# Optimization experiments

Measured on AMD Instinct MI355X. Metric: run time of the kernel, lower is better.

## Reference

```python
import jax, jax.numpy as jnp
import numpy as np

HEADS = 8
DIM_HEAD = 64
DIM_COOR = 3
SCALE = (DIM_COOR * DIM_HEAD) ** -0.5


def setup_inputs() -> dict:
    key = jax.random.key(0)
    k1, k2, k3 = jax.random.split(key, 3)
    x = jax.random.normal(k1, (2, 2048, 256, 3), dtype=jnp.float32)
    w_qkv = jax.random.normal(k2, (1536, 256), dtype=jnp.float32)
    w_out = jax.random.normal(k3, (256, 512), dtype=jnp.float32)
    return {"x": x, "w_qkv": w_qkv, "w_out": w_out}


def reference(x, w_qkv, w_out):
    b, n, _, c = x.shape
    # VNLinear: contract feature dim, keep coord dim  -> [b, n, 3*h*d, c]
    qkv = jnp.einsum('bnic,oi->bnoc', x, w_qkv)
    q, k, v = jnp.split(qkv, 3, axis=-2)  # each [b, n, h*d, c]

    def to_heads(t):
        return t.reshape(b, n, HEADS, DIM_HEAD, c).transpose(0, 2, 1, 3, 4)  # b h n d c

    q, k, v = map(to_heads, (q, k, v))
    q = q * SCALE
    # scores sum over head-dim AND coordinate-dim
    sim = jnp.einsum('bhidc,bhjdc->bhij', q, k)
    attn = jax.nn.softmax(sim, axis=-1)
    out = jnp.einsum('bhij,bhjdc->bhidc', attn, v)  # coord dim preserved
    out = out.transpose(0, 2, 1, 3, 4).reshape(b, n, HEADS * DIM_HEAD, c)
    return jnp.einsum('bnic,oi->bnoc', out, w_out)
```

## Files before the change

kernel.cpp:

```cpp
#include <hip/hip_runtime.h>
#include <hip/hip_bf16.h>

#define SCALE 0.07216878364870322f
#define LOG2E 1.4426950408889634f

typedef __bf16 bf16x8 __attribute__((ext_vector_type(8)));
typedef float f32x16 __attribute__((ext_vector_type(16)));
typedef float f32x4v __attribute__((ext_vector_type(4)));
typedef unsigned int u32x4 __attribute__((ext_vector_type(4)));
typedef unsigned short u16;

#define MFMA(a, b, c) __builtin_amdgcn_mfma_f32_32x32x16_bf16(a, b, c, 0, 0, 0)
#define MFMA16(a, b, c) __builtin_amdgcn_mfma_f32_16x16x32_bf16(a, b, c, 0, 0, 0)

__device__ __forceinline__ u16 b16(float v) { return __builtin_bit_cast(u16, (__bf16)v); }
__device__ __forceinline__ float fb16(u16 u) {
    unsigned int t = (unsigned int)u << 16;
    return __builtin_bit_cast(float, t);
}
__device__ __forceinline__ unsigned int splitpack(float v) {
    u16 h = b16(v);
    float r = v - fb16(h);
    return (unsigned int)h | ((unsigned int)b16(r) << 16);
}
__device__ __forceinline__ unsigned int pack2(float a, float b) {
    return (unsigned int)b16(a) | ((unsigned int)b16(b) << 16);
}
__device__ __forceinline__ void gload16(const void* g, void* l) {
    __builtin_amdgcn_global_load_lds((const __attribute__((address_space(1))) void*)g,
                                     (__attribute__((address_space(3))) void*)l, 16, 0, 0);
}

__global__ __launch_bounds__(256) void qkv_mfma(const float* __restrict__ x,
                                                const float* __restrict__ wq,
                                                u16* __restrict__ Qhi, u16* __restrict__ Qlo,
                                                u16* __restrict__ KVf) {
    __shared__ unsigned int ldsr[2][32][196];
    const int tid = threadIdx.x;
    const int lane = tid & 63, w = tid >> 6, hf = lane >> 5, l31 = lane & 31;
    const int lq = lane & 15, gq = lane >> 4;
    const int o0 = blockIdx.x * 64;
    const int n0 = blockIdx.y * 128;
    const int b = blockIdx.z;
    const int nw0 = n0 + w * 32;
    const int part = o0 >> 9;
    const int h = (o0 >> 6) & 7;
    const int bh = b * 8 + h;

    const float* xp = x + ((size_t)(b * 2048 + nw0 + l31)) * 768 + hf * 24;
    const float* wp0 = wq + (size_t)(o0 + l31) * 256 + hf * 8;
    const float* wp1 = wp0 + 32 * 256;

    f32x16 acc[3][2] = {};
    #pragma unroll 2
    for (int k0 = 0; k0 < 16; ++k0) {
        float xf[24], wf0[8], wf1[8];
        #pragma unroll
        for (int q = 0; q < 6; ++q) {
            f32x4v t = *(const f32x4v*)(xp + k0 * 48 + q * 4);
            xf[q * 4 + 0] = t[0]; xf[q * 4 + 1] = t[1];
            xf[q * 4 + 2] = t[2]; xf[q * 4 + 3] = t[3];
        }
        {
            f32x4v t0 = *(const f32x4v*)(wp0 + k0 * 16);
            f32x4v t1 = *(const f32x4v*)(wp0 + k0 * 16 + 4);
            f32x4v t2 = *(const f32x4v*)(wp1 + k0 * 16);
            f32x4v t3 = *(const f32x4v*)(wp1 + k0 * 16 + 4);
            #pragma unroll
            for (int e = 0; e < 4; ++e) {
                wf0[e] = t0[e]; wf0[4 + e] = t1[e];
                wf1[e] = t2[e]; wf1[4 + e] = t3[e];
            }
        }
        bf16x8 xh[3], xl[3], wh[2], wl[2];
        #pragma unroll
        for (int c = 0; c < 3; ++c)
            #pragma unroll
            for (int e = 0; e < 8; ++e) {
                float v = xf[e * 3 + c];
                __bf16 hi = (__bf16)v;
                xh[c][e] = hi;
                xl[c][e] = (__bf16)(v - (float)hi);
            }
        #pragma unroll
        for (int e = 0; e < 8; ++e) {
            { float v = wf0[e]; __bf16 hi = (__bf16)v; wh[0][e] = hi; wl[0][e] = (__bf16)(v - (float)hi); }
            { float v = wf1[e]; __bf16 hi = (__bf16)v; wh[1][e] = hi; wl[1][e] = (__bf16)(v - (float)hi); }
        }
        #pragma unroll
        for (int c = 0; c < 3; ++c)
            #pragma unroll
            for (int ot = 0; ot < 2; ++ot) {
                acc[c][ot] = MFMA(xh[c], wh[ot], acc[c][ot]);
                acc[c][ot] = MFMA(xl[c], wh[ot], acc[c][ot]);
                acc[c][ot] = MFMA(xh[c], wl[ot], acc[c][ot]);
            }
    }

    #pragma unroll
    for (int round = 0; round < 2; ++round) {
        __syncthreads();
        if ((w >> 1) == round) {
            unsigned int (*L)[196] = ldsr[w & 1];
            #pragma unroll
            for (int c = 0; c < 3; ++c)
                #pragma unroll
                for (int ot = 0; ot < 2; ++ot)
                    #pragma unroll
                    for (int r = 0; r < 16; ++r) {
                        float v = acc[c][ot][r];
                        if (part == 0) v *= (SCALE * LOG2E);
                        int nn = (r & 3) + 8 * (r >> 2) + 4 * hf;
                        int dcol = 3 * (ot * 32 + l31) + c;
                        L[nn][dcol] = (part == 2) ? (unsigned int)b16(v) : splitpack(v);
                    }
            if (part < 2) {
                #pragma unroll
                for (int is = 0; is < 2; ++is)
                    #pragma unroll
                    for (int kc = 0; kc < 6; ++kc) {
                        const unsigned int* p = &L[is * 16 + lq][kc * 32 + gq * 8];
                        u32x4 a = *(const u32x4*)p;
                        u32x4 bq = *(const u32x4*)(p + 4);
                        u32x4 hi = { (a[0] & 0xffffu) | (a[1] << 16), (a[2] & 0xffffu) | (a[3] << 16),
                                     (bq[0] & 0xffffu) | (bq[1] << 16), (bq[2] & 0xffffu) | (bq[3] << 16) };
                        u32x4 lo = { (a[0] >> 16) | (a[1] & 0xffff0000u), (a[2] >> 16) | (a[3] & 0xffff0000u),
                                     (bq[0] >> 16) | (bq[1] & 0xffff0000u), (bq[2] >> 16) | (bq[3] & 0xffff0000u) };
                        if (part == 0) {
                            size_t off = ((size_t)(bh * 128 + (nw0 >> 4) + is) * 6 + kc) * 512 + lane * 8;
                            *(u32x4*)(Qhi + off) = hi;
                            *(u32x4*)(Qlo + off) = lo;
                        } else {
                            size_t off = (size_t)(bh * 64 + (nw0 >> 5)) * 18432 + (is * 6 + kc) * 512 + lane * 8;
                            *(u32x4*)(KVf + off) = hi;
                            *(u32x4*)(KVf + off + 6144) = lo;
                        }
                    }
            } else {
                u16* vp = KVf + (size_t)(bh * 64 + (nw0 >> 5)) * 18432 + 12288 + lane * 8;
                #pragma unroll
                for (int d = 0; d < 12; ++d) {
                    unsigned int t[8];
                    #pragma unroll
                    for (int e = 0; e < 8; ++e)
                        t[e] = L[gq * 8 + e][d * 16 + lq];
                    u32x4 pk = { (t[0] & 0xffffu) | (t[1] << 16), (t[2] & 0xffffu) | (t[3] << 16),
                                 (t[4] & 0xffffu) | (t[5] << 16), (t[6] & 0xffffu) | (t[7] << 16) };
                    *(u32x4*)(vp + d * 512) = pk;
                }
            }
        }
    }
}

__global__ __launch_bounds__(256, 2) void attn_mfma(
    const u16* __restrict__ Qhi, const u16* __restrict__ Qlo,
    const u16* __restrict__ KVf, u16* __restrict__ Opart, float* __restrict__ MLp) {
    __shared__ __align__(16) u16 lds[2][18432];
    const int tid = threadIdx.x;
    const int lane = tid & 63;
    const int w = tid >> 6;
    const int g = lane >> 4;
    const int i = lane & 15;
    const int id = blockIdx.x;
    const int rem = id >> 3;
    const int grp = ((rem >> 4) << 3) | (id & 7);
    const int itile = rem & 15;
    const int bh = grp >> 1;
    const int half = grp & 1;

    bf16x8 qh[2][6], ql[2][6];
    #pragma unroll
    for (int is = 0; is < 2; ++is) {
        size_t qb = (size_t)(bh * 128 + itile * 8 + w * 2 + is) * 3072 + (size_t)lane * 8;
        #pragma unroll
        for (int kc = 0; kc < 6; ++kc) {
            qh[is][kc] = *(const bf16x8*)(Qhi + qb + kc * 512);
            ql[is][kc] = *(const bf16x8*)(Qlo + qb + kc * 512);
        }
    }

    const char* gKV = (const char*)KVf + (size_t)bh * 2359296;
    auto stage = [&](int buf, int jtAbs) {
        const char* src = gKV + (size_t)jtAbs * 36864;
        char* dst = (char*)&lds[buf][0];
        #pragma unroll
        for (int s = 0; s < 9; ++s) {
            const int c16 = (tid + s * 256) * 16;
            gload16(src + c16, dst + c16);
        }
    };

    const int jt0 = half * 32;
    stage(0, jt0);
    __syncthreads();
    int cur = 0;

    f32x4v o[2][12] = {};
    float m_run[2] = {-1e30f, -1e30f}, l_run[2] = {0.f, 0.f};

    for (int t = 0; t < 32; ++t) {
        if (t + 1 < 32) stage(cur ^ 1, jt0 + t + 1);
        const u16* L = &lds[cur][0];

        f32x4v s4[2][2] = {};
        __builtin_amdgcn_s_setprio(1);
        #pragma unroll
        for (int kc = 0; kc < 6; ++kc) {
            bf16x8 kh0 = *(const bf16x8*)&L[(unsigned)(kc * 512) + lane * 8];
            bf16x8 kh1 = *(const bf16x8*)&L[(unsigned)((6 + kc) * 512) + lane * 8];
            bf16x8 kl0 = *(const bf16x8*)&L[6144u + (unsigned)(kc * 512) + lane * 8];
            bf16x8 kl1 = *(const bf16x8*)&L[6144u + (unsigned)((6 + kc) * 512) + lane * 8];
            s4[0][0] = MFMA16(kh0, qh[0][kc], s4[0][0]);
            s4[0][1] = MFMA16(kh1, qh[0][kc], s4[0][1]);
            s4[1][0] = MFMA16(kh0, qh[1][kc], s4[1][0]);
            s4[1][1] = MFMA16(kh1, qh[1][kc], s4[1][1]);
            s4[0][0] = MFMA16(kh0, ql[0][kc], s4[0][0]);
            s4[0][1] = MFMA16(kh1, ql[0][kc], s4[0][1]);
            s4[1][0] = MFMA16(kh0, ql[1][kc], s4[1][0]);
            s4[1][1] = MFMA16(kh1, ql[1][kc], s4[1][1]);
            s4[0][0] = MFMA16(kl0, qh[0][kc], s4[0][0]);
            s4[0][1] = MFMA16(kl1, qh[0][kc], s4[0][1]);
            s4[1][0] = MFMA16(kl0, qh[1][kc], s4[1][0]);
            s4[1][1] = MFMA16(kl1, qh[1][kc], s4[1][1]);
        }
        __builtin_amdgcn_s_setprio(0);

        bf16x8 pb[2];
        #pragma unroll
        for (int is = 0; is < 2; ++is) {
            float pm = -1e30f;
            #pragma unroll
            for (int js = 0; js < 2; ++js)
                #pragma unroll
                for (int r = 0; r < 4; ++r) pm = fmaxf(pm, s4[is][js][r]);
            pm = fmaxf(pm, __shfl_xor(pm, 16, 64));
            pm = fmaxf(pm, __shfl_xor(pm, 32, 64));
            if (!__all(pm <= m_run[is] + 8.0f)) {
                float mnew = fmaxf(m_run[is], pm);
                float sc = exp2f(m_run[is] - mnew);
                l_run[is] *= sc;
                #pragma unroll
                for (int d = 0; d < 12; ++d) o[is][d] = o[is][d] * sc;
                m_run[is] = mnew;
            }
            float rs = 0.f;
            unsigned int w0[2], w1[2];
            #pragma unroll
            for (int js = 0; js < 2; ++js) {
                float p0 = exp2f(s4[is][js][0] - m_run[is]), p1 = exp2f(s4[is][js][1] - m_run[is]);
                float p2 = exp2f(s4[is][js][2] - m_run[is]), p3 = exp2f(s4[is][js][3] - m_run[is]);
                rs += (p0 + p1) + (p2 + p3);
                w0[js] = pack2(p0, p1);
                w1[js] = pack2(p2, p3);
            }
            rs += __shfl_xor(rs, 16, 64);
            rs += __shfl_xor(rs, 32, 64);
            l_run[is] += rs;

            u32x4 F;
            const int slA = ((g & 1) << 5) + i;
            const int slB = slA + 16;
            const bool ghi = (g >> 1) != 0;
            { unsigned a0 = __shfl((int)w0[0], slA, 64), a1 = __shfl((int)w0[1], slA, 64); F[0] = ghi ? a1 : a0; }
            { unsigned a0 = __shfl((int)w1[0], slA, 64), a1 = __shfl((int)w1[1], slA, 64); F[1] = ghi ? a1 : a0; }
            { unsigned a0 = __shfl((int)w0[0], slB, 64), a1 = __shfl((int)w0[1], slB, 64); F[2] = ghi ? a1 : a0; }
            { unsigned a0 = __shfl((int)w1[0], slB, 64), a1 = __shfl((int)w1[1], slB, 64); F[3] = ghi ? a1 : a0; }
            pb[is] = __builtin_bit_cast(bf16x8, F);
        }

        __builtin_amdgcn_s_setprio(1);
        #pragma unroll
        for (int d = 0; d < 12; ++d) {
            bf16x8 vf = *(const bf16x8*)&L[12288u + (unsigned)(d * 512) + lane * 8];
            o[0][d] = MFMA16(vf, pb[0], o[0][d]);
            o[1][d] = MFMA16(vf, pb[1], o[1][d]);
        }
        __builtin_amdgcn_s_setprio(0);

        if (t + 1 < 32) {
            __syncthreads();
            cur ^= 1;
        }
    }

    #pragma unroll
    for (int is = 0; is < 2; ++is) {
        const int tI = bh * 128 + itile * 8 + w * 2 + is;
        u16* Op = Opart + (size_t)(half * 2048 + tI) * 3072 + lane;
        #pragma unroll
        for (int d = 0; d < 12; ++d)
            #pragma unroll
            for (int r = 0; r < 4; ++r)
                Op[(d * 4 + r) * 64] = b16(o[is][d][r]);
        float* mlp = MLp + (size_t)(half * 2048 + tI) * 128 + lane * 2;
        mlp[0] = m_run[is];
        mlp[1] = l_run[is];
    }
}

__global__ __launch_bounds__(256) void attn_combine(const u16* __restrict__ Opart,
                                                    const float* __restrict__ MLp,
                                                    unsigned int* __restrict__ att2) {
    const int tid = threadIdx.x, lane = tid & 63, w = tid >> 6;
    const int g = lane >> 4, i = lane & 15;
    const int tI = blockIdx.x * 4 + w;
    const int bh = tI >> 7;
    const float* mla = MLp + (size_t)tI * 128 + lane * 2;
    const float* mlb = MLp + (size_t)(2048 + tI) * 128 + lane * 2;
    float ma = mla[0], la = mla[1];
    float mb = mlb[0], lb = mlb[1];
    float mm = fmaxf(ma, mb);
    float wa = exp2f(ma - mm), wb = exp2f(mb - mm);
    float inv = 1.0f / (la * wa + lb * wb);
    const u16* Oa = Opart + (size_t)tI * 3072 + lane;
    const u16* Ob = Opart + (size_t)(2048 + tI) * 3072 + lane;
    const int b2 = bh >> 3, hh = bh & 7;
    const int ig = (tI & 127) * 16 + i;
    const int itq = ig >> 5, i31 = ig & 31;
    #pragma unroll
    for (int d = 0; d < 12; ++d)
        #pragma unroll
        for (int r = 0; r < 4; ++r) {
            float va = fb16(Oa[(d * 4 + r) * 64]);
            float vb = fb16(Ob[(d * 4 + r) * 64]);
            float v = (va * wa + vb * wb) * inv;
            int dc = d * 16 + g * 4 + r;
            int dd = dc / 3, cc2 = dc - dd * 3;
            int hd = hh * 64 + dd;
            int ks = hd >> 4, e = hd & 7;
            int ln = i31 | (((hd >> 3) & 1) << 5);
            size_t off = (((size_t)(b2 * 3 + cc2) * 32 + ks) * 64 + itq) * 512 + (size_t)ln * 8 + e;
            att2[off] = splitpack(v);
        }
}

__global__ __launch_bounds__(256) void out_mfma(const unsigned int* __restrict__ att2,
                                                const float* __restrict__ wo,
                                                float* __restrict__ out) {
    const int tid = threadIdx.x, lane = tid & 63, w = tid >> 6, hf = lane >> 5, l31 = lane & 31;
    const int o0 = blockIdx.x * 32;
    const int n5 = blockIdx.y * 4 + w;
    const int b = blockIdx.z;
    const float* wp = wo + (size_t)(o0 + l31) * 512 + hf * 8;
    const unsigned int* ap = att2 + ((size_t)(b * 3) * 2048 + n5) * 512 + (size_t)lane * 8;
    f32x16 acc[3] = {};
    #pragma unroll 2
    for (int ks = 0; ks < 32; ++ks) {
        bf16x8 wh, wl;
        {
            f32x4v t0 = *(const f32x4v*)(wp + ks * 16);
            f32x4v t1 = *(const f32x4v*)(wp + ks * 16 + 4);
            #pragma unroll
            for (int e = 0; e < 4; ++e) {
                { float v = t0[e]; __bf16 hi = (__bf16)v; wh[e] = hi; wl[e] = (__bf16)(v - (float)hi); }
                { float v = t1[e]; __bf16 hi = (__bf16)v; wh[4 + e] = hi; wl[4 + e] = (__bf16)(v - (float)hi); }
            }
        }
        #pragma unroll
        for (int c = 0; c < 3; ++c) {
            const unsigned int* pc = ap + (size_t)c * 1048576 + ks * 32768;
            u32x4 a0 = *(const u32x4*)pc;
            u32x4 a1 = *(const u32x4*)(pc + 4);
            union { bf16x8 v; u32x4 u; } H, Lo;
            H.u  = { (a0[0] & 0xffffu) | (a0[1] << 16), (a0[2] & 0xffffu) | (a0[3] << 16),
                     (a1[0] & 0xffffu) | (a1[1] << 16), (a1[2] & 0xffffu) | (a1[3] << 16) };
            Lo.u = { (a0[0] >> 16) | (a0[1] & 0xffff0000u), (a0[2] >> 16) | (a0[3] & 0xffff0000u),
                     (a1[0] >> 16) | (a1[1] & 0xffff0000u), (a1[2] >> 16) | (a1[3] & 0xffff0000u) };
            acc[c] = MFMA(H.v, wh, acc[c]);
            acc[c] = MFMA(Lo.v, wh, acc[c]);
            acc[c] = MFMA(H.v, wl, acc[c]);
        }
    }
    #pragma unroll
    for (int r = 0; r < 16; ++r) {
        int n = (n5 << 5) + (r & 3) + 8 * (r >> 2) + 4 * hf;
        size_t off = ((size_t)(b * 2048 + n) * 256 + o0 + l31) * 3;
        out[off]     = acc[0][r];
        out[off + 1] = acc[1][r];
        out[off + 2] = acc[2][r];
    }
}

extern "C" void kernel_launch(void* const* d_in, const int* in_sizes, int n_in,
                              void* d_out, int out_size, void* d_ws, size_t ws_size,
                              hipStream_t stream) {
    const float* x     = (const float*)d_in[0];
    const float* w_qkv = (const float*)d_in[1];
    const float* w_out = (const float*)d_in[2];
    float* out = (float*)d_out;

    const size_t NB = (size_t)16 * 2048 * 192;
    u16* Qhi = (u16*)d_ws;
    u16* Qlo = Qhi + NB;
    u16* KVf = Qlo + NB;
    u16* Opart = KVf + (size_t)16 * 64 * 18432;
    float* MLp = (float*)(Opart + (size_t)4096 * 3072);
    unsigned int* att2 = (unsigned int*)Qhi;

    qkv_mfma<<<dim3(24, 16, 2), 256, 0, stream>>>(x, w_qkv, Qhi, Qlo, KVf);
    attn_mfma<<<dim3(512), 256, 0, stream>>>(Qhi, Qlo, KVf, Opart, MLp);
    attn_combine<<<dim3(512), 256, 0, stream>>>(Opart, MLp, att2);
    out_mfma<<<dim3(8, 16, 2), 256, 0, stream>>>(att2, w_out, out);
}
```

Before: 239.0 us.

## Fuse split-KV combine into attention kernel via in-block LDS merge

The two KV halves of each query tile now run in one 512-thread block, with four waves per half and separate double-buffered LDS regions. At the end, half 1 writes its accumulators and running max/sum into LDS, and half 0 merges them and writes the split-packed att2 layout directly. This removes the separate combine kernel, one launch, and the global round trip of bf16 partial outputs. In exchange the grid shrinks to 256 blocks using twice the LDS per block, which may reduce occupancy, and the merge uses an extra barrier with only half the waves active.

```diff
diff --git a/kernel.cpp b/kernel.cpp
--- a/kernel.cpp
+++ b/kernel.cpp
@@ -153,26 +153,25 @@
     }
 }
 
-__global__ __launch_bounds__(256, 2) void attn_mfma(
+__global__ __launch_bounds__(512, 2) void attn_mfma(
     const u16* __restrict__ Qhi, const u16* __restrict__ Qlo,
-    const u16* __restrict__ KVf, u16* __restrict__ Opart, float* __restrict__ MLp) {
-    __shared__ __align__(16) u16 lds[2][18432];
+    const u16* __restrict__ KVf, unsigned int* __restrict__ att2) {
+    __shared__ __align__(16) u16 lds[2][2][18432];
     const int tid = threadIdx.x;
     const int lane = tid & 63;
     const int w = tid >> 6;
+    const int half = w >> 2;
+    const int wl = w & 3;
     const int g = lane >> 4;
     const int i = lane & 15;
     const int id = blockIdx.x;
-    const int rem = id >> 3;
-    const int grp = ((rem >> 4) << 3) | (id & 7);
-    const int itile = rem & 15;
-    const int bh = grp >> 1;
-    const int half = grp & 1;
+    const int bh = (id & 7) * 2 + (id >> 7);
+    const int itile = (id >> 3) & 15;
 
     bf16x8 qh[2][6], ql[2][6];
     #pragma unroll
     for (int is = 0; is < 2; ++is) {
-        size_t qb = (size_t)(bh * 128 + itile * 8 + w * 2 + is) * 3072 + (size_t)lane * 8;
+        size_t qb = (size_t)(bh * 128 + itile * 8 + wl * 2 + is) * 3072 + (size_t)lane * 8;
         #pragma unroll
         for (int kc = 0; kc < 6; ++kc) {
             qh[is][kc] = *(const bf16x8*)(Qhi + qb + kc * 512);
@@ -181,12 +180,13 @@
     }
 
     const char* gKV = (const char*)KVf + (size_t)bh * 2359296;
+    const int t256 = tid & 255;
     auto stage = [&](int buf, int jtAbs) {
         const char* src = gKV + (size_t)jtAbs * 36864;
-        char* dst = (char*)&lds[buf][0];
+        char* dst = (char*)&lds[half][buf][0];
         #pragma unroll
         for (int s = 0; s < 9; ++s) {
-            const int c16 = (tid + s * 256) * 16;
+            const int c16 = (t256 + s * 256) * 16;
             gload16(src + c16, dst + c16);
         }
     };
@@ -201,7 +201,7 @@
 
     for (int t = 0; t < 32; ++t) {
         if (t + 1 < 32) stage(cur ^ 1, jt0 + t + 1);
-        const u16* L = &lds[cur][0];
+        const u16* L = &lds[half][cur][0];
 
         f32x4v s4[2][2] = {};
         __builtin_amdgcn_s_setprio(1);
@@ -284,55 +284,48 @@
         }
     }
 
-    #pragma unroll
-    for (int is = 0; is < 2; ++is) {
-        const int tI = bh * 128 + itile * 8 + w * 2 + is;
-        u16* Op = Opart + (size_t)(half * 2048 + tI) * 3072 + lane;
-        #pragma unroll
-        for (int d = 0; d < 12; ++d)
-            #pragma unroll
-            for (int r = 0; r < 4; ++r)
-                Op[(d * 4 + r) * 64] = b16(o[is][d][r]);
-        float* mlp = MLp + (size_t)(half * 2048 + tI) * 128 + lane * 2;
-        mlp[0] = m_run[is];
-        mlp[1] = l_run[is];
-    }
-}
-
-__global__ __launch_bounds__(256) void attn_combine(const u16* __restrict__ Opart,
-                                                    const float* __restrict__ MLp,
-                                                    unsigned int* __restrict__ att2) {
-    const int tid = threadIdx.x, lane = tid & 63, w = tid >> 6;
-    const int g = lane >> 4, i = lane & 15;
-    const int tI = blockIdx.x * 4 + w;
-    const int bh = tI >> 7;
-    const float* mla = MLp + (size_t)tI * 128 + lane * 2;
-    const float* mlb = MLp + (size_t)(2048 + tI) * 128 + lane * 2;
-    float ma = mla[0], la = mla[1];
-    float mb = mlb[0], lb = mlb[1];
-    float mm = fmaxf(ma, mb);
-    float wa = exp2f(ma - mm), wb = exp2f(mb - mm);
-    float inv = 1.0f / (la * wa + lb * wb);
-    const u16* Oa = Opart + (size_t)tI * 3072 + lane;
-    const u16* Ob = Opart + (size_t)(2048 + tI) * 3072 + lane;
-    const int b2 = bh >> 3, hh = bh & 7;
-    const int ig = (tI & 127) * 16 + i;
-    const int itq = ig >> 5, i31 = ig & 31;
-    #pragma unroll
-    for (int d = 0; d < 12; ++d)
-        #pragma unroll
-        for (int r = 0; r < 4; ++r) {
-            float va = fb16(Oa[(d * 4 + r) * 64]);
-            float vb = fb16(Ob[(d * 4 + r) * 64]);
-            float v = (va * wa + vb * wb) * inv;
-            int dc = d * 16 + g * 4 + r;
-            int dd = dc / 3, cc2 = dc - dd * 3;
-            int hd = hh * 64 + dd;
-            int ks = hd >> 4, e = hd & 7;
-            int ln = i31 | (((hd >> 3) & 1) << 5);
-            size_t off = (((size_t)(b2 * 3 + cc2) * 32 + ks) * 64 + itq) * 512 + (size_t)ln * 8 + e;
-            att2[off] = splitpack(v);
-        }
+    float* LM = (float*)&lds[0][0][0];
+    __syncthreads();
+    if (half == 1) {
+        #pragma unroll
+        for (int is = 0; is < 2; ++is) {
+            #pragma unroll
+            for (int d = 0; d < 12; ++d)
+                *(f32x4v*)&LM[(((wl * 2 + is) * 12 + d) * 64 + lane) * 4] = o[is][d];
+            LM[24576 + ((wl * 2 + is) * 64 + lane) * 2 + 0] = m_run[is];
+            LM[24576 + ((wl * 2 + is) * 64 + lane) * 2 + 1] = l_run[is];
+        }
+    }
+    __syncthreads();
+    if (half == 0) {
+        const int b2 = bh >> 3, hh = bh & 7;
+        #pragma unroll
+        for (int is = 0; is < 2; ++is) {
+            float mb = LM[24576 + ((wl * 2 + is) * 64 + lane) * 2 + 0];
+            float lb = LM[24576 + ((wl * 2 + is) * 64 + lane) * 2 + 1];
+            float mm = fmaxf(m_run[is], mb);
+            float wa = exp2f(m_run[is] - mm);
+            float wb = exp2f(mb - mm);
+            float inv = 1.0f / (l_run[is] * wa + lb * wb);
+            const int ig = (itile * 8 + wl * 2 + is) * 16 + i;
+            const int itq = ig >> 5, i31 = ig & 31;
+            #pragma unroll
+            for (int d = 0; d < 12; ++d) {
+                f32x4v vb = *(const f32x4v*)&LM[(((wl * 2 + is) * 12 + d) * 64 + lane) * 4];
+                #pragma unroll
+                for (int r = 0; r < 4; ++r) {
+                    float v = (o[is][d][r] * wa + vb[r] * wb) * inv;
+                    int dc = d * 16 + g * 4 + r;
+                    int dd = dc / 3, cc2 = dc - dd * 3;
+                    int hd = hh * 64 + dd;
+                    int ks = hd >> 4, e = hd & 7;
+                    int ln = i31 | (((hd >> 3) & 1) << 5);
+                    size_t off = (((size_t)(b2 * 3 + cc2) * 32 + ks) * 64 + itq) * 512 + (size_t)ln * 8 + e;
+                    att2[off] = splitpack(v);
+                }
+            }
+        }
+    }
 }
 
 __global__ __launch_bounds__(256) void out_mfma(const unsigned int* __restrict__ att2,
@@ -391,15 +384,13 @@
     float* out = (float*)d_out;
 
     const size_t NB = (size_t)16 * 2048 * 192;
+    const size_t KVN = (size_t)16 * 64 * 18432;
     u16* Qhi = (u16*)d_ws;
     u16* Qlo = Qhi + NB;
     u16* KVf = Qlo + NB;
-    u16* Opart = KVf + (size_t)16 * 64 * 18432;
-    float* MLp = (float*)(Opart + (size_t)4096 * 3072);
-    unsigned int* att2 = (unsigned int*)Qhi;
+    unsigned int* att2 = (unsigned int*)(KVf + KVN);
 
     qkv_mfma<<<dim3(24, 16, 2), 256, 0, stream>>>(x, w_qkv, Qhi, Qlo, KVf);
-    attn_mfma<<<dim3(512), 256, 0, stream>>>(Qhi, Qlo, KVf, Opart, MLp);
-    attn_combine<<<dim3(512), 256, 0, stream>>>(Opart, MLp, att2);
+    attn_mfma<<<dim3(256), 512, 0, stream>>>(Qhi, Qlo, KVf, att2);
     out_mfma<<<dim3(8, 16, 2), 256, 0, stream>>>(att2, w_out, out);
 }
```

New measurement: 234.4 us. No clear change (-1.9%).
